# Kernel tuning notes

Hardware: AMD Instinct MI355X
Metric: run time of the kernel (lower is better)

Reference implementation:

```python
import jax, jax.numpy as jnp
import numpy as np

D, H, DH, L, F, NM = 512, 8, 64, 8, 2048, 80
B, S = 8, 1024


def _ln(x, g, b, eps=1e-5):
    mu = x.mean(-1, keepdims=True)
    var = ((x - mu) ** 2).mean(-1, keepdims=True)
    return (x - mu) / jnp.sqrt(var + eps) * g + b


def setup_inputs() -> dict:
    key = jax.random.key(0)
    ks = jax.random.split(key, 16)
    n = lambda k, sh: jax.random.normal(k, sh, dtype=jnp.float32) * 0.02
    # sinusoidal positional encoding, as in PositionalEncoding
    pos = np.arange(S, dtype=np.float32)[:, None]
    div = np.exp(np.arange(0, D, 2, dtype=np.float32) * (-np.log(10000.0) / D))
    pe = np.zeros((S, D), dtype=np.float32)
    pe[:, 0::2] = np.sin(pos * div)
    pe[:, 1::2] = np.cos(pos * div)
    return dict(
        mel=jax.random.normal(ks[0], (B, S, NM), dtype=jnp.float32),
        pe=jnp.asarray(pe),
        proj_w=n(ks[1], (NM, D)), proj_b=jnp.zeros((D,), jnp.float32),
        Wq=n(ks[2], (L, D, D)), bq=jnp.zeros((L, D), jnp.float32),
        Wk=n(ks[3], (L, D, D)), bk=jnp.zeros((L, D), jnp.float32),
        Wv=n(ks[4], (L, D, D)), bv=jnp.zeros((L, D), jnp.float32),
        Wo=n(ks[5], (L, D, D)), bo=jnp.zeros((L, D), jnp.float32),
        ln1_g=jnp.ones((L, D), jnp.float32), ln1_b=jnp.zeros((L, D), jnp.float32),
        ln2_g=jnp.ones((L, D), jnp.float32), ln2_b=jnp.zeros((L, D), jnp.float32),
        Wi=n(ks[6], (L, D, F)), bi=jnp.zeros((L, F), jnp.float32),
        Wf=n(ks[7], (L, F, D)), bf=jnp.zeros((L, D), jnp.float32),
        lnf_g=jnp.ones((D,), jnp.float32), lnf_b=jnp.zeros((D,), jnp.float32),
        lang_w=n(ks[8], (D, 100)), lang_b=jnp.zeros((100,), jnp.float32),
        int_w=n(ks[9], (D, 50)), int_b=jnp.zeros((50,), jnp.float32),
        emo_w=n(ks[10], (D, 8)), emo_b=jnp.zeros((8,), jnp.float32),
        sp_w=n(ks[11], (D, 1000)), sp_b=jnp.zeros((1000,), jnp.float32),
    )


def reference(mel, pe, proj_w, proj_b, Wq, bq, Wk, bk, Wv, bv, Wo, bo,
              ln1_g, ln1_b, ln2_g, ln2_b, Wi, bi, Wf, bf,
              lnf_g, lnf_b, lang_w, lang_b, int_w, int_b, emo_w, emo_b, sp_w, sp_b):
    # feature extraction projection + positional encoding
    h = mel @ proj_w + proj_b + pe[None]  # (B, S, D)
    scale = 1.0 / np.sqrt(DH)

    def block(h, p):
        wq, bq_, wk, bk_, wv, bv_, wo, bo_, g1, b1, g2, b2, wi, bi_, wf, bf_ = p
        x = _ln(h, g1, b1)
        b, s, _ = x.shape
        heads = lambda y, w, bias: (y @ w + bias).reshape(b, s, H, DH).transpose(0, 2, 1, 3)
        q, k, v = heads(x, wq, bq_), heads(x, wk, bk_), heads(x, wv, bv_)
        probs = jax.nn.softmax(jnp.einsum('bhqd,bhkd->bhqk', q, k) * scale, axis=-1)
        ctx = jnp.einsum('bhqk,bhkd->bhqd', probs, v).transpose(0, 2, 1, 3).reshape(b, s, D)
        h = h + ctx @ wo + bo_
        y = _ln(h, g2, b2)
        h = h + jax.nn.gelu(y @ wi + bi_, approximate=False) @ wf + bf_
        return h, None

    h, _ = jax.lax.scan(block, h, (Wq, bq, Wk, bk, Wv, bv, Wo, bo,
                                   ln1_g, ln1_b, ln2_g, ln2_b, Wi, bi, Wf, bf))
    h = _ln(h, lnf_g, lnf_b)
    pooled = h.mean(axis=1)  # no mask: sequence_lengths=None path
    language_logits = pooled @ lang_w + lang_b
    intent_logits = pooled @ int_w + int_b
    emotion_logits = pooled @ emo_w + emo_b
    speech_logits = h @ sp_w + sp_b
    return (language_logits, intent_logits, emotion_logits, speech_logits)
```

## Files before the change

kernel.cpp:

```cpp
#include <hip/hip_runtime.h>
#include <hip/hip_bf16.h>
#include <math.h>

#define DD   512
#define HH   8
#define DHH  64
#define LL   8
#define FF   2048
#define NMEL 80
#define BB   8
#define SS   1024
#define MM   (BB*SS)

typedef __attribute__((ext_vector_type(8))) short bf16x8;
typedef __attribute__((ext_vector_type(4))) float f32x4;
typedef __attribute__((ext_vector_type(4))) unsigned short u16x4;

#define GLOAD_LDS16(g, l) __builtin_amdgcn_global_load_lds( \
    (const __attribute__((address_space(1))) void*)(g),      \
    (__attribute__((address_space(3))) void*)(l), 16, 0, 0)

__device__ __forceinline__ unsigned short f2bf(float x) {
    __hip_bfloat16 b = __float2bfloat16(x);
    return *reinterpret_cast<unsigned short*>(&b);
}

__global__ __launch_bounds__(256) void proj_pe_kernel(
    const float* __restrict__ mel, const float* __restrict__ pw,
    const float* __restrict__ pb, const float* __restrict__ pe,
    float* __restrict__ h)
{
    int row = blockIdx.x;
    int s = row & (SS - 1);
    __shared__ float m_s[NMEL];
    int t = threadIdx.x;
    if (t < NMEL) m_s[t] = mel[(size_t)row * NMEL + t];
    __syncthreads();
    for (int d = t; d < DD; d += 256) {
        float acc = pb[d] + pe[(size_t)s * DD + d];
        #pragma unroll 8
        for (int k = 0; k < NMEL; ++k)
            acc = fmaf(m_s[k], pw[(size_t)k * DD + d], acc);
        h[(size_t)row * DD + d] = acc;
    }
}

__global__ __launch_bounds__(256) void ln_kernel(
    const float* __restrict__ in, const float* __restrict__ g,
    const float* __restrict__ bta, __hip_bfloat16* __restrict__ out)
{
    int row = blockIdx.x;
    const float* xr = in + (size_t)row * DD;
    int t = threadIdx.x;
    float x0 = xr[t], x1 = xr[t + 256];
    float s = x0 + x1;
    float ss = x0 * x0 + x1 * x1;
    #pragma unroll
    for (int off = 32; off; off >>= 1) {
        s  += __shfl_down(s, off);
        ss += __shfl_down(ss, off);
    }
    __shared__ float red1[4], red2[4];
    int lane = t & 63, w = t >> 6;
    if (lane == 0) { red1[w] = s; red2[w] = ss; }
    __syncthreads();
    s  = red1[0] + red1[1] + red1[2] + red1[3];
    ss = red2[0] + red2[1] + red2[2] + red2[3];
    float mu  = s * (1.f / DD);
    float var = ss * (1.f / DD) - mu * mu;
    float rstd = rsqrtf(var + 1e-5f);
    out[(size_t)row * DD + t]       = __float2bfloat16((x0 - mu) * rstd * g[t]       + bta[t]);
    out[(size_t)row * DD + t + 256] = __float2bfloat16((x1 - mu) * rstd * g[t + 256] + bta[t + 256]);
}

__global__ __launch_bounds__(256) void wconv_kernel(
    const float* __restrict__ in, __hip_bfloat16* __restrict__ out,
    int K, int N, int rstride, int rowoff)
{
    __shared__ float tile[32][33];
    size_t lin  = (size_t)blockIdx.z * K * N;
    size_t lout = (size_t)blockIdx.z * rstride * K + (size_t)rowoff * K;
    int tx = threadIdx.x & 31, ty = threadIdx.x >> 5;
    int n0 = blockIdx.x * 32, k0 = blockIdx.y * 32;
    #pragma unroll
    for (int i = 0; i < 32; i += 8) {
        int k = k0 + ty + i, n = n0 + tx;
        tile[ty + i][tx] = (n < N) ? in[lin + (size_t)k * N + n] : 0.f;
    }
    __syncthreads();
    #pragma unroll
    for (int i = 0; i < 32; i += 8) {
        int n = n0 + ty + i, k = k0 + tx;
        out[lout + (size_t)n * K + k] = __float2bfloat16(tile[tx][ty + i]);
    }
}

template<int OUTMODE, bool GELU_EP, bool RESID>
__global__ __launch_bounds__(512) void gemm_bf16(
    const __hip_bfloat16* __restrict__ A,
    const __hip_bfloat16* __restrict__ Bt,
    const float* __restrict__ b0, const float* __restrict__ b1,
    const float* __restrict__ b2,
    const float* __restrict__ resid,
    float* __restrict__ Cf,
    __hip_bfloat16* __restrict__ O0, __hip_bfloat16* __restrict__ O1,
    __hip_bfloat16* __restrict__ O2,
    int M, int N, int K)
{
    __shared__ __align__(16) __hip_bfloat16 As[128 * 64];
    __shared__ __align__(16) __hip_bfloat16 Bs[128 * 64];
    int t = threadIdx.x;
    int w = t >> 6, lane = t & 63, g = lane >> 4, li = lane & 15;
    int wm = w >> 2, wn = w & 3;
    size_t bm = (size_t)blockIdx.y * 128;
    size_t bn = (size_t)blockIdx.x * 128;

    const f32x4 vzero = {0.f, 0.f, 0.f, 0.f};
    f32x4 acc[4][2];
    #pragma unroll
    for (int i = 0; i < 4; ++i)
        #pragma unroll
        for (int j = 0; j < 2; ++j) acc[i][j] = vzero;

    for (int k0 = 0; k0 < K; k0 += 64) {
        #pragma unroll
        for (int i = 0; i < 2; ++i) {
            int c = i * 512 + t;
            int row = c >> 3, col = (c & 7) << 3;
            GLOAD_LDS16(A + (bm + row) * (size_t)K + k0 + col, As + (size_t)c * 8);
        }
        #pragma unroll
        for (int i = 0; i < 2; ++i) {
            int c = i * 512 + t;
            int row = c >> 3, col = (c & 7) << 3;
            GLOAD_LDS16(Bt + (bn + row) * (size_t)K + k0 + col, Bs + (size_t)c * 8);
        }
        __syncthreads();
        #pragma unroll
        for (int kk = 0; kk < 2; ++kk) {
            bf16x8 af[4], bfr[2];
            #pragma unroll
            for (int mi = 0; mi < 4; ++mi)
                af[mi] = *reinterpret_cast<const bf16x8*>(As + (wm * 64 + mi * 16 + li) * 64 + kk * 32 + g * 8);
            #pragma unroll
            for (int ni = 0; ni < 2; ++ni)
                bfr[ni] = *reinterpret_cast<const bf16x8*>(Bs + (wn * 32 + ni * 16 + li) * 64 + kk * 32 + g * 8);
            #pragma unroll
            for (int mi = 0; mi < 4; ++mi)
                #pragma unroll
                for (int ni = 0; ni < 2; ++ni)
                    acc[mi][ni] = __builtin_amdgcn_mfma_f32_16x16x32_bf16(af[mi], bfr[ni], acc[mi][ni], 0, 0, 0);
        }
        __syncthreads();
    }

    #pragma unroll
    for (int mi = 0; mi < 4; ++mi) {
        #pragma unroll
        for (int ni = 0; ni < 2; ++ni) {
            f32x4 v = acc[mi][ni];
            int coll = wn * 32 + ni * 16 + li;
            size_t col = bn + coll;
            if ((int)col >= N) continue;
            float bv;
            int sel = 0, c = (int)col;
            if (OUTMODE == 2) {
                sel = (int)(col >> 9); c = (int)(col & 511);
                bv = (sel == 0) ? b0[c] : (sel == 1) ? b1[c] : b2[c];
            } else {
                bv = b0[col];
            }
            #pragma unroll
            for (int r = 0; r < 4; ++r) {
                size_t row = bm + wm * 64 + mi * 16 + g * 4 + r;
                float x = v[r] + bv;
                if (GELU_EP) x = 0.5f * x * (1.f + erff(x * 0.70710678118654752440f));
                if (RESID)   x += resid[row * (size_t)N + col];
                if (OUTMODE == 0) {
                    Cf[row * (size_t)N + col] = x;
                } else if (OUTMODE == 1) {
                    O0[row * (size_t)N + col] = __float2bfloat16(x);
                } else {
                    size_t b = row >> 10, s = row & (SS - 1);
                    size_t h = (size_t)(c >> 6), d = (size_t)(c & 63);
                    __hip_bfloat16 xb = __float2bfloat16(x);
                    if (sel == 0)      O0[((b * HH + h) << 16) + (s << 6) + d] = xb;
                    else if (sel == 1) O1[((b * HH + h) << 16) + (s << 6) + d] = xb;
                    else               O2[((b * HH + h) << 16) + (d << 10) + s] = xb;
                }
            }
        }
    }
}

__global__ __launch_bounds__(512, 4) void attn_mfma(
    const __hip_bfloat16* __restrict__ qb,
    const __hip_bfloat16* __restrict__ kb,
    const __hip_bfloat16* __restrict__ vtb,
    __hip_bfloat16* __restrict__ ctx)
{
    __shared__ __align__(16) char smem[49152];
    unsigned short (*Plds)[32][40] = (unsigned short (*)[32][40])smem;
    float* comb = (float*)smem;

    int t = threadIdx.x;
    int w = t >> 6, lane = t & 63, g = lane >> 4, li = lane & 15;
    int wq = w & 3, wk = w >> 2;
    int bh = blockIdx.y;
    int b = bh >> 3, h = bh & 7;
    int q0 = blockIdx.x * 128 + wq * 32;

    const __hip_bfloat16* Qp = qb  + ((size_t)bh << 16);
    const __hip_bfloat16* Kp = kb  + ((size_t)bh << 16);
    const __hip_bfloat16* Vp = vtb + ((size_t)bh << 16);

    bf16x8 qf[2][2];
    #pragma unroll
    for (int qt = 0; qt < 2; ++qt)
        #pragma unroll
        for (int kk = 0; kk < 2; ++kk)
            qf[qt][kk] = *reinterpret_cast<const bf16x8*>(
                Qp + (size_t)(q0 + qt * 16 + li) * DHH + kk * 32 + g * 8);

    const f32x4 vzero = {0.f, 0.f, 0.f, 0.f};
    f32x4 acc_oT[2][4];
    float m_r[2], l_r[2];
    #pragma unroll
    for (int qt = 0; qt < 2; ++qt) {
        #pragma unroll
        for (int dt = 0; dt < 4; ++dt) acc_oT[qt][dt] = vzero;
        m_r[qt] = -1e30f; l_r[qt] = 0.f;
    }

    const float csc = 0.125f * 1.44269504088896340736f;

    for (int it = 0; it < 16; ++it) {
        int ks0 = wk * 512 + it * 32;
        f32x4 accs[2][2];
        #pragma unroll
        for (int qt = 0; qt < 2; ++qt)
            #pragma unroll
            for (int kt = 0; kt < 2; ++kt) accs[qt][kt] = vzero;
        #pragma unroll
        for (int kk = 0; kk < 2; ++kk) {
            bf16x8 kf[2];
            #pragma unroll
            for (int kt = 0; kt < 2; ++kt)
                kf[kt] = *reinterpret_cast<const bf16x8*>(
                    Kp + (size_t)(ks0 + kt * 16 + li) * DHH + kk * 32 + g * 8);
            #pragma unroll
            for (int qt = 0; qt < 2; ++qt)
                #pragma unroll
                for (int kt = 0; kt < 2; ++kt)
                    accs[qt][kt] = __builtin_amdgcn_mfma_f32_16x16x32_bf16(kf[kt], qf[qt][kk], accs[qt][kt], 0, 0, 0);
        }

        float mnew[2];
        #pragma unroll
        for (int qt = 0; qt < 2; ++qt) {
            float a0 = fmaxf(fmaxf(accs[qt][0][0], accs[qt][0][1]),
                             fmaxf(accs[qt][0][2], accs[qt][0][3]));
            float a1 = fmaxf(fmaxf(accs[qt][1][0], accs[qt][1][1]),
                             fmaxf(accs[qt][1][2], accs[qt][1][3]));
            float m = fmaxf(a0, a1);
            m = fmaxf(m, __shfl_xor(m, 16));
            m = fmaxf(m, __shfl_xor(m, 32));
            mnew[qt] = m * csc;
        }

        bool grow = (mnew[0] > m_r[0] + 11.0f) || (mnew[1] > m_r[1] + 11.0f);
        if (__any(grow)) {
            #pragma unroll
            for (int qt = 0; qt < 2; ++qt) {
                float mn = fmaxf(m_r[qt], mnew[qt]);
                float alpha = exp2f(m_r[qt] - mn);
                m_r[qt] = mn;
                l_r[qt] *= alpha;
                #pragma unroll
                for (int dt = 0; dt < 4; ++dt)
                    #pragma unroll
                    for (int r = 0; r < 4; ++r)
                        acc_oT[qt][dt][r] *= alpha;
            }
        }

        float rs[2] = {0.f, 0.f};
        #pragma unroll
        for (int qt = 0; qt < 2; ++qt) {
            #pragma unroll
            for (int kt = 0; kt < 2; ++kt) {
                u16x4 pk;
                #pragma unroll
                for (int r = 0; r < 4; ++r) {
                    float p = exp2f(fmaf(accs[qt][kt][r], csc, -m_r[qt]));
                    rs[qt] += p;
                    pk[r] = f2bf(p);
                }
                *reinterpret_cast<u16x4*>(&Plds[w][qt * 16 + li][kt * 16 + g * 4]) = pk;
            }
            float s = rs[qt];
            s += __shfl_xor(s, 16);
            s += __shfl_xor(s, 32);
            l_r[qt] += s;
        }

        __builtin_amdgcn_wave_barrier();

        bf16x8 pf[2];
        #pragma unroll
        for (int qt = 0; qt < 2; ++qt)
            pf[qt] = *reinterpret_cast<const bf16x8*>(&Plds[w][qt * 16 + li][g * 8]);
        #pragma unroll
        for (int dt = 0; dt < 4; ++dt) {
            bf16x8 vf = *reinterpret_cast<const bf16x8*>(
                Vp + (size_t)(dt * 16 + li) * SS + ks0 + g * 8);
            #pragma unroll
            for (int qt = 0; qt < 2; ++qt)
                acc_oT[qt][dt] = __builtin_amdgcn_mfma_f32_16x16x32_bf16(vf, pf[qt], acc_oT[qt][dt], 0, 0, 0);
        }
        __builtin_amdgcn_wave_barrier();
    }

    __syncthreads();
    if (wk == 1) {
        float* cb = comb + ((size_t)(w - 4) * 64 + lane) * 36;
        #pragma unroll
        for (int qt = 0; qt < 2; ++qt)
            #pragma unroll
            for (int dt = 0; dt < 4; ++dt)
                *reinterpret_cast<f32x4*>(cb + qt * 16 + dt * 4) = acc_oT[qt][dt];
        #pragma unroll
        for (int qt = 0; qt < 2; ++qt) {
            cb[32 + qt] = m_r[qt];
            cb[34 + qt] = l_r[qt];
        }
    }
    __syncthreads();
    if (wk == 0) {
        float* cb = comb + ((size_t)w * 64 + lane) * 36;
        #pragma unroll
        for (int qt = 0; qt < 2; ++qt) {
            float m2 = cb[32 + qt];
            float l2 = cb[34 + qt];
            float mg = fmaxf(m_r[qt], m2);
            float a1 = exp2f(m_r[qt] - mg);
            float a2 = exp2f(m2 - mg);
            float inv = 1.f / (l_r[qt] * a1 + l2 * a2);
            int q = q0 + qt * 16 + li;
            #pragma unroll
            for (int dt = 0; dt < 4; ++dt) {
                f32x4 ob = *reinterpret_cast<const f32x4*>(cb + qt * 16 + dt * 4);
                u16x4 pk;
                #pragma unroll
                for (int r = 0; r < 4; ++r)
                    pk[r] = f2bf((acc_oT[qt][dt][r] * a1 + ob[r] * a2) * inv);
                *reinterpret_cast<u16x4*>(
                    &ctx[((size_t)(b * SS + q)) * DD + h * DHH + dt * 16 + g * 4]) = pk;
            }
        }
    }
}

__global__ __launch_bounds__(512) void pool_kernel(
    const __hip_bfloat16* __restrict__ hf, float* __restrict__ pooled)
{
    int b = blockIdx.x;
    int d = threadIdx.x;
    float acc = 0.f;
    for (int s = 0; s < SS; ++s)
        acc += __bfloat162float(hf[((size_t)(b * SS + s)) * DD + d]);
    pooled[b * DD + d] = acc * (1.f / SS);
}

__global__ __launch_bounds__(256) void heads_kernel(
    const float* __restrict__ pooled,
    const float* __restrict__ lw, const float* __restrict__ lb,
    const float* __restrict__ iw, const float* __restrict__ ib,
    const float* __restrict__ ew, const float* __restrict__ eb,
    float* __restrict__ out)
{
    int b = blockIdx.x;
    __shared__ float ps[DD];
    int t = threadIdx.x;
    ps[t] = pooled[b * DD + t];
    ps[t + 256] = pooled[b * DD + t + 256];
    __syncthreads();
    if (t < 158) {
        const float* wptr; const float* bptr; float* optr; int n; int j;
        if (t < 100)      { j = t;       wptr = lw; bptr = lb; optr = out;        n = 100; }
        else if (t < 150) { j = t - 100; wptr = iw; bptr = ib; optr = out + 800;  n = 50;  }
        else              { j = t - 150; wptr = ew; bptr = eb; optr = out + 1200; n = 8;   }
        float acc = bptr[j];
        for (int k2 = 0; k2 < DD; ++k2)
            acc = fmaf(ps[k2], wptr[(size_t)k2 * n + j], acc);
        optr[b * n + j] = acc;
    }
}

extern "C" void kernel_launch(void* const* d_in, const int* in_sizes, int n_in,
                              void* d_out, int out_size, void* d_ws, size_t ws_size,
                              hipStream_t stream)
{
    const float* mel    = (const float*)d_in[0];
    const float* pe     = (const float*)d_in[1];
    const float* proj_w = (const float*)d_in[2];
    const float* proj_b = (const float*)d_in[3];
    const float* Wq     = (const float*)d_in[4];
    const float* bq     = (const float*)d_in[5];
    const float* Wk     = (const float*)d_in[6];
    const float* bk     = (const float*)d_in[7];
    const float* Wv     = (const float*)d_in[8];
    const float* bv     = (const float*)d_in[9];
    const float* Wo     = (const float*)d_in[10];
    const float* bo     = (const float*)d_in[11];
    const float* ln1_g  = (const float*)d_in[12];
    const float* ln1_b  = (const float*)d_in[13];
    const float* ln2_g  = (const float*)d_in[14];
    const float* ln2_b  = (const float*)d_in[15];
    const float* Wi     = (const float*)d_in[16];
    const float* bi     = (const float*)d_in[17];
    const float* Wf     = (const float*)d_in[18];
    const float* bf     = (const float*)d_in[19];
    const float* lnf_g  = (const float*)d_in[20];
    const float* lnf_b  = (const float*)d_in[21];
    const float* lang_w = (const float*)d_in[22];
    const float* lang_b = (const float*)d_in[23];
    const float* int_w  = (const float*)d_in[24];
    const float* int_b  = (const float*)d_in[25];
    const float* emo_w  = (const float*)d_in[26];
    const float* emo_b  = (const float*)d_in[27];
    const float* sp_w   = (const float*)d_in[28];
    const float* sp_b   = (const float*)d_in[29];

    float* out = (float*)d_out;
    char* wsb = (char*)d_ws;

    const size_t MB = 1ull << 20;
    float* hbuf           = (float*)(wsb);
    __hip_bfloat16* xb    = (__hip_bfloat16*)(wsb + 16 * MB);
    __hip_bfloat16* qbuf  = (__hip_bfloat16*)(wsb + 24 * MB);
    __hip_bfloat16* kbuf  = (__hip_bfloat16*)(wsb + 32 * MB);
    __hip_bfloat16* vtb   = (__hip_bfloat16*)(wsb + 40 * MB);
    __hip_bfloat16* ctx   = (__hip_bfloat16*)(wsb + 48 * MB);
    __hip_bfloat16* gbuf  = (__hip_bfloat16*)(wsb + 24 * MB);
    float* pooled         = (float*)(wsb + 56 * MB);
    __hip_bfloat16* wqkv  = (__hip_bfloat16*)(wsb + 57 * MB);
    __hip_bfloat16* wot   = (__hip_bfloat16*)(wsb + 70 * MB);
    __hip_bfloat16* wit   = (__hip_bfloat16*)(wsb + 74 * MB);
    __hip_bfloat16* wft   = (__hip_bfloat16*)(wsb + 90 * MB);
    __hip_bfloat16* spt   = (__hip_bfloat16*)(wsb + 107 * MB);

    wconv_kernel<<<dim3(16, 16, LL), 256, 0, stream>>>(Wq, wqkv, DD, DD, 1536, 0);
    wconv_kernel<<<dim3(16, 16, LL), 256, 0, stream>>>(Wk, wqkv, DD, DD, 1536, 512);
    wconv_kernel<<<dim3(16, 16, LL), 256, 0, stream>>>(Wv, wqkv, DD, DD, 1536, 1024);
    wconv_kernel<<<dim3(16, 16, LL), 256, 0, stream>>>(Wo, wot, DD, DD, DD, 0);
    wconv_kernel<<<dim3(64, 16, LL), 256, 0, stream>>>(Wi, wit, DD, FF, FF, 0);
    wconv_kernel<<<dim3(16, 64, LL), 256, 0, stream>>>(Wf, wft, FF, DD, DD, 0);
    wconv_kernel<<<dim3(32, 16, 1),  256, 0, stream>>>(sp_w, spt, DD, 1000, 1024, 0);

    proj_pe_kernel<<<MM, 256, 0, stream>>>(mel, proj_w, proj_b, pe, hbuf);

    dim3 g512(4, 64);

    for (int l = 0; l < LL; ++l) {
        const __hip_bfloat16* wqkv_l = wqkv + (size_t)l * 1536 * DD;
        const __hip_bfloat16* wot_l  = wot  + (size_t)l * DD * DD;
        const __hip_bfloat16* wit_l  = wit  + (size_t)l * FF * DD;
        const __hip_bfloat16* wft_l  = wft  + (size_t)l * DD * FF;

        ln_kernel<<<MM, 256, 0, stream>>>(hbuf, ln1_g + l * DD, ln1_b + l * DD, xb);

        gemm_bf16<2, false, false><<<dim3(12, 64), 512, 0, stream>>>(
            xb, wqkv_l, bq + l * DD, bk + l * DD, bv + l * DD,
            nullptr, nullptr, qbuf, kbuf, vtb, MM, 1536, DD);

        attn_mfma<<<dim3(SS / 128, BB * HH), 512, 0, stream>>>(qbuf, kbuf, vtb, ctx);

        gemm_bf16<0, false, true><<<g512, 512, 0, stream>>>(
            ctx, wot_l, bo + l * DD, nullptr, nullptr,
            hbuf, hbuf, nullptr, nullptr, nullptr, MM, DD, DD);

        ln_kernel<<<MM, 256, 0, stream>>>(hbuf, ln2_g + l * DD, ln2_b + l * DD, xb);

        gemm_bf16<1, true, false><<<dim3(16, 64), 512, 0, stream>>>(
            xb, wit_l, bi + l * FF, nullptr, nullptr,
            nullptr, nullptr, gbuf, nullptr, nullptr, MM, FF, DD);
        gemm_bf16<0, false, true><<<g512, 512, 0, stream>>>(
            gbuf, wft_l, bf + l * DD, nullptr, nullptr,
            hbuf, hbuf, nullptr, nullptr, nullptr, MM, DD, FF);
    }

    ln_kernel<<<MM, 256, 0, stream>>>(hbuf, lnf_g, lnf_b, xb);
    pool_kernel<<<BB, 512, 0, stream>>>(xb, pooled);
    heads_kernel<<<BB, 256, 0, stream>>>(pooled, lang_w, lang_b, int_w, int_b,
                                         emo_w, emo_b, out);

    gemm_bf16<0, false, false><<<dim3(8, 64), 512, 0, stream>>>(
        xb, spt, sp_b, nullptr, nullptr,
        nullptr, out + 1264, nullptr, nullptr, nullptr, MM, 1000, DD);
}
```

Before: 1.885 ms.

## Use wave-per-row vectorized LayerNorm and XCD-aware block swizzles for GEMM and attention

Measured after the change: 1.800 ms. 4.5% less time.

```diff
diff --git a/kernel.cpp b/kernel.cpp
--- a/kernel.cpp
+++ b/kernel.cpp
@@ -15,6 +15,7 @@
 typedef __attribute__((ext_vector_type(8))) short bf16x8;
 typedef __attribute__((ext_vector_type(4))) float f32x4;
 typedef __attribute__((ext_vector_type(4))) unsigned short u16x4;
+typedef __attribute__((ext_vector_type(8))) unsigned short u16x8;
 
 #define GLOAD_LDS16(g, l) __builtin_amdgcn_global_load_lds( \
     (const __attribute__((address_space(1))) void*)(g),      \
@@ -45,32 +46,38 @@
     }
 }
 
-__global__ __launch_bounds__(256) void ln_kernel(
+__global__ __launch_bounds__(512) void ln_kernel(
     const float* __restrict__ in, const float* __restrict__ g,
     const float* __restrict__ bta, __hip_bfloat16* __restrict__ out)
 {
-    int row = blockIdx.x;
-    const float* xr = in + (size_t)row * DD;
-    int t = threadIdx.x;
-    float x0 = xr[t], x1 = xr[t + 256];
-    float s = x0 + x1;
-    float ss = x0 * x0 + x1 * x1;
-    #pragma unroll
-    for (int off = 32; off; off >>= 1) {
-        s  += __shfl_down(s, off);
-        ss += __shfl_down(ss, off);
-    }
-    __shared__ float red1[4], red2[4];
-    int lane = t & 63, w = t >> 6;
-    if (lane == 0) { red1[w] = s; red2[w] = ss; }
-    __syncthreads();
-    s  = red1[0] + red1[1] + red1[2] + red1[3];
-    ss = red2[0] + red2[1] + red2[2] + red2[3];
+    int w = threadIdx.x >> 6, lane = threadIdx.x & 63;
+    int row = blockIdx.x * 8 + w;
+    const float4* xr = reinterpret_cast<const float4*>(in + (size_t)row * DD) + lane * 2;
+    float4 v0 = xr[0], v1 = xr[1];
+    float s  = v0.x + v0.y + v0.z + v0.w + v1.x + v1.y + v1.z + v1.w;
+    float ss = v0.x*v0.x + v0.y*v0.y + v0.z*v0.z + v0.w*v0.w
+             + v1.x*v1.x + v1.y*v1.y + v1.z*v1.z + v1.w*v1.w;
+    #pragma unroll
+    for (int off = 1; off < 64; off <<= 1) {
+        s  += __shfl_xor(s, off);
+        ss += __shfl_xor(ss, off);
+    }
     float mu  = s * (1.f / DD);
     float var = ss * (1.f / DD) - mu * mu;
     float rstd = rsqrtf(var + 1e-5f);
-    out[(size_t)row * DD + t]       = __float2bfloat16((x0 - mu) * rstd * g[t]       + bta[t]);
-    out[(size_t)row * DD + t + 256] = __float2bfloat16((x1 - mu) * rstd * g[t + 256] + bta[t + 256]);
+    const float4* gp = reinterpret_cast<const float4*>(g) + lane * 2;
+    const float4* bp = reinterpret_cast<const float4*>(bta) + lane * 2;
+    float4 g0 = gp[0], g1 = gp[1], b0 = bp[0], b1 = bp[1];
+    u16x8 o;
+    o[0] = f2bf((v0.x - mu) * rstd * g0.x + b0.x);
+    o[1] = f2bf((v0.y - mu) * rstd * g0.y + b0.y);
+    o[2] = f2bf((v0.z - mu) * rstd * g0.z + b0.z);
+    o[3] = f2bf((v0.w - mu) * rstd * g0.w + b0.w);
+    o[4] = f2bf((v1.x - mu) * rstd * g1.x + b1.x);
+    o[5] = f2bf((v1.y - mu) * rstd * g1.y + b1.y);
+    o[6] = f2bf((v1.z - mu) * rstd * g1.z + b1.z);
+    o[7] = f2bf((v1.w - mu) * rstd * g1.w + b1.w);
+    *reinterpret_cast<u16x8*>(out + (size_t)row * DD + lane * 8) = o;
 }
 
 __global__ __launch_bounds__(256) void wconv_kernel(
@@ -112,8 +119,14 @@
     int t = threadIdx.x;
     int w = t >> 6, lane = t & 63, g = lane >> 4, li = lane & 15;
     int wm = w >> 2, wn = w & 3;
-    size_t bm = (size_t)blockIdx.y * 128;
-    size_t bn = (size_t)blockIdx.x * 128;
+
+    int nwg = gridDim.x * gridDim.y;
+    int lin = blockIdx.y * gridDim.x + blockIdx.x;
+    int xcd = lin & 7, idx = lin >> 3;
+    int q8 = nwg >> 3, r8 = nwg & 7;
+    int swz = (xcd < r8 ? xcd * (q8 + 1) : r8 * (q8 + 1) + (xcd - r8) * q8) + idx;
+    size_t bm = (size_t)(swz / gridDim.x) * 128;
+    size_t bn = (size_t)(swz % gridDim.x) * 128;
 
     const f32x4 vzero = {0.f, 0.f, 0.f, 0.f};
     f32x4 acc[4][2];
@@ -206,9 +219,9 @@
     int t = threadIdx.x;
     int w = t >> 6, lane = t & 63, g = lane >> 4, li = lane & 15;
     int wq = w & 3, wk = w >> 2;
-    int bh = blockIdx.y;
+    int bh = blockIdx.x;
     int b = bh >> 3, h = bh & 7;
-    int q0 = blockIdx.x * 128 + wq * 32;
+    int q0 = blockIdx.y * 128 + wq * 32;
 
     const __hip_bfloat16* Qp = qb  + ((size_t)bh << 16);
     const __hip_bfloat16* Kp = kb  + ((size_t)bh << 16);
@@ -468,19 +481,19 @@
         const __hip_bfloat16* wit_l  = wit  + (size_t)l * FF * DD;
         const __hip_bfloat16* wft_l  = wft  + (size_t)l * DD * FF;
 
-        ln_kernel<<<MM, 256, 0, stream>>>(hbuf, ln1_g + l * DD, ln1_b + l * DD, xb);
+        ln_kernel<<<MM / 8, 512, 0, stream>>>(hbuf, ln1_g + l * DD, ln1_b + l * DD, xb);
 
         gemm_bf16<2, false, false><<<dim3(12, 64), 512, 0, stream>>>(
             xb, wqkv_l, bq + l * DD, bk + l * DD, bv + l * DD,
             nullptr, nullptr, qbuf, kbuf, vtb, MM, 1536, DD);
 
-        attn_mfma<<<dim3(SS / 128, BB * HH), 512, 0, stream>>>(qbuf, kbuf, vtb, ctx);
+        attn_mfma<<<dim3(BB * HH, SS / 128), 512, 0, stream>>>(qbuf, kbuf, vtb, ctx);
 
         gemm_bf16<0, false, true><<<g512, 512, 0, stream>>>(
             ctx, wot_l, bo + l * DD, nullptr, nullptr,
             hbuf, hbuf, nullptr, nullptr, nullptr, MM, DD, DD);
 
-        ln_kernel<<<MM, 256, 0, stream>>>(hbuf, ln2_g + l * DD, ln2_b + l * DD, xb);
+        ln_kernel<<<MM / 8, 512, 0, stream>>>(hbuf, ln2_g + l * DD, ln2_b + l * DD, xb);
 
         gemm_bf16<1, true, false><<<dim3(16, 64), 512, 0, stream>>>(
             xb, wit_l, bi + l * FF, nullptr, nullptr,
@@ -490,7 +503,7 @@
             hbuf, hbuf, nullptr, nullptr, nullptr, MM, DD, FF);
     }
 
-    ln_kernel<<<MM, 256, 0, stream>>>(hbuf, lnf_g, lnf_b, xb);
+    ln_kernel<<<MM / 8, 512, 0, stream>>>(hbuf, lnf_g, lnf_b, xb);
     pool_kernel<<<BB, 512, 0, stream>>>(xb, pooled);
     heads_kernel<<<BB, 256, 0, stream>>>(pooled, lang_w, lang_b, int_w, int_b,
                                          emo_w, emo_b, out);
```
